# Kernel tuning notes

Measured on AMD Instinct MI355X. Metric: run time of the kernel, lower is better.

## Reference

```python
import jax, jax.numpy as jnp
import numpy as np

D_MODEL = 1024
NHEAD = 16
D_K = D_MODEL // NHEAD


def setup_inputs() -> dict:
    key = jax.random.key(0)
    ks = jax.random.split(key, 11)
    B, S = 2, 2048
    scale = 1.0 / np.sqrt(D_MODEL)
    inp = {
        "q": jax.random.normal(ks[0], (B, S, D_MODEL), jnp.float32),
        "k": jax.random.normal(ks[1], (B, S, D_MODEL), jnp.float32),
        "v": jax.random.normal(ks[2], (B, S, D_MODEL), jnp.float32),
        "Wq": jax.random.normal(ks[3], (D_MODEL, D_MODEL), jnp.float32) * scale,
        "bq": jnp.zeros((D_MODEL,), jnp.float32),
        "Wk": jax.random.normal(ks[4], (D_MODEL, D_MODEL), jnp.float32) * scale,
        "bk": jnp.zeros((D_MODEL,), jnp.float32),
        "Wv": jax.random.normal(ks[5], (D_MODEL, D_MODEL), jnp.float32) * scale,
        "bv": jnp.zeros((D_MODEL,), jnp.float32),
        "Wo": jax.random.normal(ks[6], (D_MODEL, D_MODEL), jnp.float32) * scale,
        "bo": jnp.zeros((D_MODEL,), jnp.float32),
    }
    return inp


def reference(q, k, v, Wq, bq, Wk, bk, Wv, bv, Wo, bo):
    B, S, _ = q.shape
    # Linear projections (torch Linear: x @ W.T + b), split into heads
    def proj(x, W, b):
        y = jnp.einsum('bsd,ed->bse', x, W) + b
        return y.reshape(B, -1, NHEAD, D_K).transpose(0, 2, 1, 3)  # [B,H,S,Dk]

    qh = proj(q, Wq, bq)
    kh = proj(k, Wk, bk)
    vh = proj(v, Wv, bv)

    scores = jnp.einsum('bhqd,bhkd->bhqk', qh, kh) / jnp.sqrt(
        jnp.asarray(D_K, qh.dtype))
    attn = jax.nn.softmax(scores, axis=-1)  # dropout is identity in eval
    out = jnp.einsum('bhqk,bhkd->bhqd', attn, vh)
    out = out.transpose(0, 2, 1, 3).reshape(B, S, D_MODEL)
    return jnp.einsum('bsd,ed->bse', out, Wo) + bo
```

## Files before the change

kernel.cpp:

```cpp
#include <hip/hip_runtime.h>
#include <stdint.h>
#include <stddef.h>

#define D_MODEL 1024
#define NHEAD   16
#define DK      64
#define BB      2
#define SS      2048
#define NTOK    (BB*SS)

#define SCALE_Q 0.18033688011f

typedef short  short8 __attribute__((ext_vector_type(8)));
typedef __bf16 bf16x8 __attribute__((ext_vector_type(8)));
typedef float  f32x4  __attribute__((ext_vector_type(4)));

__device__ __forceinline__ unsigned short f2bf(float x){
  unsigned int u = __builtin_bit_cast(unsigned int, x);
  u += 0x7fffu + ((u >> 16) & 1u);
  return (unsigned short)(u >> 16);
}

__device__ __forceinline__ unsigned int pack_bf2(float x, float y){
  unsigned int a = __builtin_bit_cast(unsigned int, x) + 0x8000u;
  unsigned int b = __builtin_bit_cast(unsigned int, y) + 0x8000u;
  return __builtin_amdgcn_perm(b, a, 0x07060302u);
}

__device__ __forceinline__ unsigned int cvt_pk_bf16(float lo, float hi){
  unsigned int r;
  asm("v_cvt_pk_bf16_f32 %0, %1, %2" : "=v"(r) : "v"(lo), "v"(hi));
  return r;
}

__device__ __forceinline__ float fast_exp2(float x){
#if __has_builtin(__builtin_amdgcn_exp2f)
  return __builtin_amdgcn_exp2f(x);
#else
  return exp2f(x);
#endif
}

__device__ __forceinline__ f32x4 mfma16(bf16x8 a, bf16x8 b, f32x4 c){
  return __builtin_amdgcn_mfma_f32_16x16x32_bf16(a, b, c, 0, 0, 0);
}

__device__ __forceinline__ void async16(const void* g, void* lds){
  __builtin_amdgcn_global_load_lds(
      (const __attribute__((address_space(1))) unsigned int*)g,
      (__attribute__((address_space(3))) unsigned int*)lds,
      16, 0, 0);
}

__global__ __launch_bounds__(256) void cast_bf16_all(
    const float* __restrict__ q,  const float* __restrict__ k,  const float* __restrict__ v,
    const float* __restrict__ wq, const float* __restrict__ wk, const float* __restrict__ wv,
    const float* __restrict__ wo,
    unsigned short* __restrict__ qb,  unsigned short* __restrict__ kb,  unsigned short* __restrict__ vb,
    unsigned short* __restrict__ wqb, unsigned short* __restrict__ wkb, unsigned short* __restrict__ wvb,
    unsigned short* __restrict__ wob)
{
  const float* src; unsigned short* dst; int n;
  switch (blockIdx.y){
    case 0: src = q;  dst = qb;  n = NTOK*D_MODEL;    break;
    case 1: src = k;  dst = kb;  n = NTOK*D_MODEL;    break;
    case 2: src = v;  dst = vb;  n = NTOK*D_MODEL;    break;
    case 3: src = wq; dst = wqb; n = D_MODEL*D_MODEL; break;
    case 4: src = wk; dst = wkb; n = D_MODEL*D_MODEL; break;
    case 5: src = wv; dst = wvb; n = D_MODEL*D_MODEL; break;
    default: src = wo; dst = wob; n = D_MODEL*D_MODEL; break;
  }
  int i = (blockIdx.x * 256 + threadIdx.x) * 8;
  if (i >= n) return;
  float4 a = *(const float4*)(src + i);
  float4 b = *(const float4*)(src + i + 4);
  short8 o;
  o[0] = (short)f2bf(a.x); o[1] = (short)f2bf(a.y);
  o[2] = (short)f2bf(a.z); o[3] = (short)f2bf(a.w);
  o[4] = (short)f2bf(b.x); o[5] = (short)f2bf(b.y);
  o[6] = (short)f2bf(b.z); o[7] = (short)f2bf(b.w);
  *(short8*)(dst + i) = o;
}

__global__ __launch_bounds__(256) void qkv_gemm(
    const unsigned short* __restrict__ qb, const unsigned short* __restrict__ kb,
    const unsigned short* __restrict__ vb,
    const unsigned short* __restrict__ wqb, const unsigned short* __restrict__ wkb,
    const unsigned short* __restrict__ wvb,
    const float* __restrict__ bq, const float* __restrict__ bk, const float* __restrict__ bv,
    unsigned short* __restrict__ Qh, unsigned short* __restrict__ Kh, unsigned short* __restrict__ Vt)
{
  __shared__ __align__(16) unsigned short As[128*64];
  __shared__ __align__(16) unsigned short Bs[128*64];
  const int id = blockIdx.x, z = id >> 8, r = id & 255;
  const unsigned short *A, *Bt; const float* bias; unsigned short* C;
  int bm, bn, N, brow; float scale;
  if (z == 0){ A = qb;  Bt = wqb; bias = bq; C = Qh; bm = (r>>3)*128; bn = (r&7)*128; N = 1024; brow = 0; scale = SCALE_Q; }
  else if (z == 1){ A = kb;  Bt = wkb; bias = bk; C = Kh; bm = (r>>3)*128; bn = (r&7)*128; N = 1024; brow = 0; scale = 1.0f; }
  else            { A = wvb; Bt = vb;  bias = bv; C = Vt; bm = (r&7)*128; bn = (r>>3)*128; N = 4096; brow = 1; scale = 1.0f; }
  const int K = 1024;
  const int tid  = threadIdx.x, lane = tid & 63, w = tid >> 6;
  const int quad = lane >> 4,   l16  = lane & 15;
  const int wm = w >> 1, wn = w & 1;
  const int sw = l16 & 7;
  f32x4 acc[4][4] = {};
  for (int kb_ = 0; kb_ < 16; ++kb_){
    const int k0 = kb_ << 6;
    __syncthreads();
    #pragma unroll
    for (int c = 0; c < 4; ++c){
      int chunk = (w*4 + c)*64 + lane;
      int row = chunk >> 3, c8 = chunk & 7;
      int cs = (c8 ^ (row & 7)) << 3;
      async16(A  + (size_t)(bm + row)*K + k0 + cs, (char*)As + (w*4 + c)*1024);
      async16(Bt + (size_t)(bn + row)*K + k0 + cs, (char*)Bs + (w*4 + c)*1024);
    }
    __syncthreads();
    bf16x8 af[4][2], bf[4][2];
    #pragma unroll
    for (int mt = 0; mt < 4; ++mt)
      #pragma unroll
      for (int ks = 0; ks < 2; ++ks){
        int off = (((ks*4 + quad) ^ sw) << 3);
        af[mt][ks] = *(const bf16x8*)&As[(wm*64 + mt*16 + l16)*64 + off];
        bf[mt][ks] = *(const bf16x8*)&Bs[(wn*64 + mt*16 + l16)*64 + off];
      }
    #pragma unroll
    for (int ks = 0; ks < 2; ++ks)
      #pragma unroll
      for (int mt = 0; mt < 4; ++mt)
        #pragma unroll
        for (int nt = 0; nt < 4; ++nt)
          acc[mt][nt] = mfma16(af[mt][ks], bf[nt][ks], acc[mt][nt]);
  }
  const int m0 = bm + wm*64, n0 = bn + wn*64;
  #pragma unroll
  for (int mt = 0; mt < 4; ++mt){
    #pragma unroll
    for (int nt = 0; nt < 4; ++nt){
      int col = n0 + nt*16 + l16;
      float bc = brow ? 0.0f : bias[col];
      #pragma unroll
      for (int rr = 0; rr < 4; ++rr){
        int row = m0 + mt*16 + quad*4 + rr;
        float val = (acc[mt][nt][rr] + (brow ? bias[row] : bc)) * scale;
        C[(size_t)row*N + col] = f2bf(val);
      }
    }
  }
}

__global__ __launch_bounds__(256) void gemm_out(
    const unsigned short* __restrict__ A, const unsigned short* __restrict__ Bt,
    const float* __restrict__ bias, float* __restrict__ C)
{
  __shared__ __align__(16) unsigned short As[64*64];
  __shared__ __align__(16) unsigned short Bs[128*64];
  const int K = 1024, N = 1024;
  const int tid  = threadIdx.x, lane = tid & 63, w = tid >> 6;
  const int quad = lane >> 4,   l16  = lane & 15;
  const int bm = blockIdx.y * 64, bn = blockIdx.x * 128;
  const int sw = l16 & 7;
  f32x4 acc[4][2] = {};
  for (int kb_ = 0; kb_ < 16; ++kb_){
    const int k0 = kb_ << 6;
    __syncthreads();
    #pragma unroll
    for (int c = 0; c < 2; ++c){
      int chunk = (w*2 + c)*64 + lane;
      int row = chunk >> 3, c8 = chunk & 7;
      async16(A + (size_t)(bm + row)*K + k0 + ((c8 ^ (row & 7)) << 3),
              (char*)As + (w*2 + c)*1024);
    }
    #pragma unroll
    for (int c = 0; c < 4; ++c){
      int chunk = (w*4 + c)*64 + lane;
      int row = chunk >> 3, c8 = chunk & 7;
      async16(Bt + (size_t)(bn + row)*K + k0 + ((c8 ^ (row & 7)) << 3),
              (char*)Bs + (w*4 + c)*1024);
    }
    __syncthreads();
    bf16x8 af[4][2], bf[2][2];
    #pragma unroll
    for (int mt = 0; mt < 4; ++mt)
      #pragma unroll
      for (int ks = 0; ks < 2; ++ks)
        af[mt][ks] = *(const bf16x8*)&As[(mt*16 + l16)*64 + (((ks*4 + quad) ^ sw) << 3)];
    #pragma unroll
    for (int nt = 0; nt < 2; ++nt)
      #pragma unroll
      for (int ks = 0; ks < 2; ++ks)
        bf[nt][ks] = *(const bf16x8*)&Bs[(w*32 + nt*16 + l16)*64 + (((ks*4 + quad) ^ sw) << 3)];
    #pragma unroll
    for (int ks = 0; ks < 2; ++ks)
      #pragma unroll
      for (int mt = 0; mt < 4; ++mt)
        #pragma unroll
        for (int nt = 0; nt < 2; ++nt)
          acc[mt][nt] = mfma16(af[mt][ks], bf[nt][ks], acc[mt][nt]);
  }
  #pragma unroll
  for (int mt = 0; mt < 4; ++mt){
    #pragma unroll
    for (int nt = 0; nt < 2; ++nt){
      int col = bn + w*32 + nt*16 + l16;
      float bc = bias[col];
      #pragma unroll
      for (int rr = 0; rr < 4; ++rr){
        int row = bm + mt*16 + quad*4 + rr;
        C[(size_t)row*N + col] = acc[mt][nt][rr] + bc;
      }
    }
  }
}

__global__ __launch_bounds__(256) void attn(
    const unsigned short* __restrict__ Qh, const unsigned short* __restrict__ Kh,
    const unsigned short* __restrict__ Vt, unsigned short* __restrict__ ctx)
{
  __shared__ __align__(16) unsigned short Kbuf[2][64*64];
  __shared__ __align__(16) unsigned short Vbuf[2][64*64];
  __shared__ __align__(16) unsigned short QP[128*64];

  const int tid  = threadIdx.x, lane = tid & 63, w = tid >> 6;
  const int quad = lane >> 4,   l16  = lane & 15;
  const int b = blockIdx.y >> 4, h = blockIdx.y & 15;
  const int q0 = blockIdx.x * 128;
  const int sw = l16 & 7;
  const int qh = quad >> 1, ql = (quad & 1) * 4;

  #pragma unroll
  for (int c = 0; c < 4; ++c){
    int s = (w*4 + c)*64 + lane;
    int row = s >> 3, c8 = s & 7;
    async16(Qh + (size_t)(b*SS + q0 + row)*D_MODEL + h*DK + ((c8 ^ (row & 7)) << 3),
            (char*)QP + (w*4 + c)*1024);
  }

  const unsigned short* Kp = Kh + (size_t)(b*SS)*D_MODEL + h*DK;
  const unsigned short* Vp = Vt + (size_t)(h*DK)*NTOK + b*SS;
  const unsigned short* ksrc[2];
  const unsigned short* vsrc[2];
  #pragma unroll
  for (int c = 0; c < 2; ++c){
    int s = (w*2 + c)*64 + lane;
    int row = s >> 3, c8 = s & 7;
    int cs = (c8 ^ (row & 7)) << 3;
    ksrc[c] = Kp + (size_t)row*D_MODEL + cs;
    vsrc[c] = Vp + (size_t)row*NTOK  + cs;
  }

  #pragma unroll
  for (int c = 0; c < 2; ++c){
    async16(ksrc[c], (char*)Kbuf[0] + (w*2 + c)*1024);
    async16(vsrc[c], (char*)Vbuf[0] + (w*2 + c)*1024);
    ksrc[c] += 64*D_MODEL;
    vsrc[c] += 64;
  }
  __syncthreads();

  bf16x8 bq0[2], bq1[2];
  #pragma unroll
  for (int ks = 0; ks < 2; ++ks){
    bq0[ks] = *(const bf16x8*)&QP[(w*32 +      l16)*64 + (((ks*4 + quad) ^ sw) << 3)];
    bq1[ks] = *(const bf16x8*)&QP[(w*32 + 16 + l16)*64 + (((ks*4 + quad) ^ sw) << 3)];
  }

  f32x4 acc[2][4] = {};
  float l_i[2] = {0.0f, 0.0f};

  for (int it = 0; it < 32; ++it){
    const int cur = it & 1;
    #pragma unroll
    for (int c = 0; c < 2; ++c){
      async16(ksrc[c], (char*)Kbuf[1 - cur] + (w*2 + c)*1024);
      async16(vsrc[c], (char*)Vbuf[1 - cur] + (w*2 + c)*1024);
      ksrc[c] += 64*D_MODEL;
      vsrc[c] += 64;
    }
    asm volatile("s_waitcnt vmcnt(4)\n\ts_barrier" ::: "memory");

    const unsigned short* Kc = Kbuf[cur];
    const unsigned short* Vc = Vbuf[cur];

    bf16x8 kf[4][2];
    #pragma unroll
    for (int mt = 0; mt < 4; ++mt)
      #pragma unroll
      for (int ks = 0; ks < 2; ++ks)
        kf[mt][ks] = *(const bf16x8*)&Kc[(mt*16 + l16)*64 + (((ks*4 + quad) ^ sw) << 3)];

    uint2 vfr[4][2][2];
    #pragma unroll
    for (int nt = 0; nt < 4; ++nt)
      #pragma unroll
      for (int ks = 0; ks < 2; ++ks){
        int rb = (nt*16 + l16)*64 + ql;
        vfr[nt][ks][0] = *(const uint2*)&Vc[rb + (((ks*4     + qh) ^ sw) << 3)];
        vfr[nt][ks][1] = *(const uint2*)&Vc[rb + (((ks*4 + 2 + qh) ^ sw) << 3)];
      }

    f32x4 s0[4] = {}, s1[4] = {};
    #pragma unroll
    for (int mt = 0; mt < 4; ++mt)
      #pragma unroll
      for (int ks = 0; ks < 2; ++ks){
        s0[mt] = mfma16(kf[mt][ks], bq0[ks], s0[mt]);
        s1[mt] = mfma16(kf[mt][ks], bq1[ks], s1[mt]);
      }

    float ls0 = 0.0f, ls1 = 0.0f;
    #pragma unroll
    for (int mt = 0; mt < 4; ++mt)
      #pragma unroll
      for (int rr = 0; rr < 4; ++rr){
        float p0 = fast_exp2(s0[mt][rr]); s0[mt][rr] = p0; ls0 += p0;
        float p1 = fast_exp2(s1[mt][rr]); s1[mt][rr] = p1; ls1 += p1;
      }
    l_i[0] += ls0; l_i[1] += ls1;

    bf16x8 bp0[2], bp1[2];
    #pragma unroll
    for (int ks = 0; ks < 2; ++ks){
      uint4 t;
      t.x = cvt_pk_bf16(s0[2*ks  ][0], s0[2*ks  ][1]);
      t.y = cvt_pk_bf16(s0[2*ks  ][2], s0[2*ks  ][3]);
      t.z = cvt_pk_bf16(s0[2*ks+1][0], s0[2*ks+1][1]);
      t.w = cvt_pk_bf16(s0[2*ks+1][2], s0[2*ks+1][3]);
      bp0[ks] = __builtin_bit_cast(bf16x8, t);
      t.x = cvt_pk_bf16(s1[2*ks  ][0], s1[2*ks  ][1]);
      t.y = cvt_pk_bf16(s1[2*ks  ][2], s1[2*ks  ][3]);
      t.z = cvt_pk_bf16(s1[2*ks+1][0], s1[2*ks+1][1]);
      t.w = cvt_pk_bf16(s1[2*ks+1][2], s1[2*ks+1][3]);
      bp1[ks] = __builtin_bit_cast(bf16x8, t);
    }

    #pragma unroll
    for (int nt = 0; nt < 4; ++nt)
      #pragma unroll
      for (int ks = 0; ks < 2; ++ks){
        uint4 vv;
        vv.x = vfr[nt][ks][0].x; vv.y = vfr[nt][ks][0].y;
        vv.z = vfr[nt][ks][1].x; vv.w = vfr[nt][ks][1].y;
        bf16x8 vf = __builtin_bit_cast(bf16x8, vv);
        acc[0][nt] = mfma16(vf, bp0[ks], acc[0][nt]);
        acc[1][nt] = mfma16(vf, bp1[ks], acc[1][nt]);
      }

    asm volatile("s_waitcnt lgkmcnt(0)\n\ts_barrier" ::: "memory");
  }

  float inv[2];
  #pragma unroll
  for (int qg = 0; qg < 2; ++qg){
    float t = l_i[qg];
    t += __shfl_xor(t, 16);
    t += __shfl_xor(t, 32);
    inv[qg] = 1.0f / t;
  }
  #pragma unroll
  for (int qg = 0; qg < 2; ++qg){
    int pr = (w*32 + qg*16 + l16)*64;
    #pragma unroll
    for (int nt = 0; nt < 4; ++nt){
      int c8  = nt*2 + (quad >> 1);
      int off = ((c8 ^ sw) << 3) + (quad & 1)*4;
      uint2 p;
      p.x = pack_bf2(acc[qg][nt][0]*inv[qg], acc[qg][nt][1]*inv[qg]);
      p.y = pack_bf2(acc[qg][nt][2]*inv[qg], acc[qg][nt][3]*inv[qg]);
      *(uint2*)&QP[pr + off] = p;
    }
  }
  asm volatile("s_waitcnt lgkmcnt(0)" ::: "memory");
  {
    int r  = w*32 + (lane >> 1);
    int j0 = (lane & 1)*4;
    unsigned short* dst = ctx + (size_t)(b*SS + q0 + r)*D_MODEL + h*DK;
    #pragma unroll
    for (int i = 0; i < 4; ++i){
      int j = j0 + i;
      uint4 d = *(const uint4*)&QP[r*64 + ((j ^ (r & 7)) << 3)];
      *(uint4*)(dst + j*8) = d;
    }
  }
}

extern "C" void kernel_launch(void* const* d_in, const int* in_sizes, int n_in,
                              void* d_out, int out_size, void* d_ws, size_t ws_size,
                              hipStream_t stream) {
  const float* q  = (const float*)d_in[0];
  const float* k  = (const float*)d_in[1];
  const float* v  = (const float*)d_in[2];
  const float* Wq = (const float*)d_in[3];
  const float* bq = (const float*)d_in[4];
  const float* Wk = (const float*)d_in[5];
  const float* bk = (const float*)d_in[6];
  const float* Wv = (const float*)d_in[7];
  const float* bv = (const float*)d_in[8];
  const float* Wo = (const float*)d_in[9];
  const float* bo = (const float*)d_in[10];

  char* ws = (char*)d_ws;
  const size_t TOKB = (size_t)NTOK * D_MODEL * 2;
  const size_t WB   = (size_t)D_MODEL * D_MODEL * 2;
  unsigned short* qb  = (unsigned short*)ws;             ws += TOKB;
  unsigned short* kb  = (unsigned short*)ws;             ws += TOKB;
  unsigned short* vb  = (unsigned short*)ws;             ws += TOKB;
  unsigned short* wqb = (unsigned short*)ws;             ws += WB;
  unsigned short* wkb = (unsigned short*)ws;             ws += WB;
  unsigned short* wvb = (unsigned short*)ws;             ws += WB;
  unsigned short* wob = (unsigned short*)ws;             ws += WB;
  unsigned short* Qh  = (unsigned short*)ws;             ws += TOKB;
  unsigned short* Kh  = (unsigned short*)ws;             ws += TOKB;
  unsigned short* Vt  = (unsigned short*)ws;             ws += TOKB;
  unsigned short* ctx = (unsigned short*)ws;             ws += TOKB;

  cast_bf16_all<<<dim3(2048, 7), 256, 0, stream>>>(q, k, v, Wq, Wk, Wv, Wo,
                                                   qb, kb, vb, wqb, wkb, wvb, wob);
  qkv_gemm<<<dim3(768), 256, 0, stream>>>(qb, kb, vb, wqb, wkb, wvb,
                                          bq, bk, bv, Qh, Kh, Vt);
  attn<<<dim3(SS/128, BB*NHEAD), 256, 0, stream>>>(Qh, Kh, Vt, ctx);
  gemm_out<<<dim3(8, 64), 256, 0, stream>>>(ctx, wob, bo, (float*)d_out);
}
```

Baseline: 239.6 us.

## Double KV tile to 128 keys per stage with new V swizzle and MFMA priority

Each pipeline stage of the attention kernel now loads 128 keys instead of 64 and processes them as two halves, cutting the main loop to 16 iterations. This halves the barriers and waitcnt stalls per key. The V buffer layout and its XOR swizzle are reworked for 128-wide rows. The MFMA sections are wrapped in s_setprio, and the row-sum accumulators are split to shorten dependency chains. The cost is double the LDS use for K/V buffers, which may reduce occupancy.

```diff
diff --git a/kernel.cpp b/kernel.cpp
--- a/kernel.cpp
+++ b/kernel.cpp
@@ -218,16 +218,16 @@
     const unsigned short* __restrict__ Qh, const unsigned short* __restrict__ Kh,
     const unsigned short* __restrict__ Vt, unsigned short* __restrict__ ctx)
 {
-  __shared__ __align__(16) unsigned short Kbuf[2][64*64];
-  __shared__ __align__(16) unsigned short Vbuf[2][64*64];
+  __shared__ __align__(16) unsigned short Kbuf[2][128*64];
+  __shared__ __align__(16) unsigned short Vbuf[2][64*128];
   __shared__ __align__(16) unsigned short QP[128*64];
 
   const int tid  = threadIdx.x, lane = tid & 63, w = tid >> 6;
   const int quad = lane >> 4,   l16  = lane & 15;
   const int b = blockIdx.y >> 4, h = blockIdx.y & 15;
   const int q0 = blockIdx.x * 128;
-  const int sw = l16 & 7;
-  const int qh = quad >> 1, ql = (quad & 1) * 4;
+  const int sw   = l16 & 7;
+  const int vkey = l16 & 14;
 
   #pragma unroll
   for (int c = 0; c < 4; ++c){
@@ -239,23 +239,23 @@
 
   const unsigned short* Kp = Kh + (size_t)(b*SS)*D_MODEL + h*DK;
   const unsigned short* Vp = Vt + (size_t)(h*DK)*NTOK + b*SS;
-  const unsigned short* ksrc[2];
-  const unsigned short* vsrc[2];
-  #pragma unroll
-  for (int c = 0; c < 2; ++c){
-    int s = (w*2 + c)*64 + lane;
-    int row = s >> 3, c8 = s & 7;
-    int cs = (c8 ^ (row & 7)) << 3;
-    ksrc[c] = Kp + (size_t)row*D_MODEL + cs;
-    vsrc[c] = Vp + (size_t)row*NTOK  + cs;
-  }
-
-  #pragma unroll
-  for (int c = 0; c < 2; ++c){
-    async16(ksrc[c], (char*)Kbuf[0] + (w*2 + c)*1024);
-    async16(vsrc[c], (char*)Vbuf[0] + (w*2 + c)*1024);
-    ksrc[c] += 64*D_MODEL;
-    vsrc[c] += 64;
+  const unsigned short* ksrc[4];
+  const unsigned short* vsrc[4];
+  #pragma unroll
+  for (int c = 0; c < 4; ++c){
+    int s = (w*4 + c)*64 + lane;
+    int kr = s >> 3, kc8 = s & 7;
+    ksrc[c] = Kp + (size_t)kr*D_MODEL + ((kc8 ^ (kr & 7)) << 3);
+    int vr = s >> 4, vc16 = s & 15;
+    vsrc[c] = Vp + (size_t)vr*NTOK + ((vc16 ^ ((vr >> 1) & 7)) << 3);
+  }
+
+  #pragma unroll
+  for (int c = 0; c < 4; ++c){
+    async16(ksrc[c], (char*)Kbuf[0] + (w*4 + c)*1024);
+    async16(vsrc[c], (char*)Vbuf[0] + (w*4 + c)*1024);
+    ksrc[c] += 128*D_MODEL;
+    vsrc[c] += 128;
   }
   __syncthreads();
 
@@ -267,89 +267,99 @@
   }
 
   f32x4 acc[2][4] = {};
-  float l_i[2] = {0.0f, 0.0f};
-
-  for (int it = 0; it < 32; ++it){
+  float l0a = 0.0f, l0b = 0.0f, l1a = 0.0f, l1b = 0.0f;
+
+  for (int it = 0; it < 16; ++it){
     const int cur = it & 1;
     #pragma unroll
-    for (int c = 0; c < 2; ++c){
-      async16(ksrc[c], (char*)Kbuf[1 - cur] + (w*2 + c)*1024);
-      async16(vsrc[c], (char*)Vbuf[1 - cur] + (w*2 + c)*1024);
-      ksrc[c] += 64*D_MODEL;
-      vsrc[c] += 64;
-    }
-    asm volatile("s_waitcnt vmcnt(4)\n\ts_barrier" ::: "memory");
+    for (int c = 0; c < 4; ++c){
+      async16(ksrc[c], (char*)Kbuf[1 - cur] + (w*4 + c)*1024);
+      async16(vsrc[c], (char*)Vbuf[1 - cur] + (w*4 + c)*1024);
+      ksrc[c] += 128*D_MODEL;
+      vsrc[c] += 128;
+    }
+    asm volatile("s_waitcnt vmcnt(8)\n\ts_barrier" ::: "memory");
 
     const unsigned short* Kc = Kbuf[cur];
     const unsigned short* Vc = Vbuf[cur];
 
-    bf16x8 kf[4][2];
-    #pragma unroll
-    for (int mt = 0; mt < 4; ++mt)
-      #pragma unroll
-      for (int ks = 0; ks < 2; ++ks)
-        kf[mt][ks] = *(const bf16x8*)&Kc[(mt*16 + l16)*64 + (((ks*4 + quad) ^ sw) << 3)];
-
-    uint2 vfr[4][2][2];
-    #pragma unroll
-    for (int nt = 0; nt < 4; ++nt)
-      #pragma unroll
-      for (int ks = 0; ks < 2; ++ks){
-        int rb = (nt*16 + l16)*64 + ql;
-        vfr[nt][ks][0] = *(const uint2*)&Vc[rb + (((ks*4     + qh) ^ sw) << 3)];
-        vfr[nt][ks][1] = *(const uint2*)&Vc[rb + (((ks*4 + 2 + qh) ^ sw) << 3)];
+    #pragma unroll
+    for (int half = 0; half < 2; ++half){
+      bf16x8 kf[4][2];
+      #pragma unroll
+      for (int mt = 0; mt < 4; ++mt)
+        #pragma unroll
+        for (int ks = 0; ks < 2; ++ks)
+          kf[mt][ks] = *(const bf16x8*)&Kc[(half*64 + mt*16 + l16)*64 + (((ks*4 + quad) ^ sw) << 3)];
+
+      uint2 vfr[4][2][2];
+      #pragma unroll
+      for (int nt = 0; nt < 4; ++nt)
+        #pragma unroll
+        for (int kss = 0; kss < 2; ++kss){
+          int rb = (nt*16 + l16)*128;
+          int hd = 8*(2*half + kss) + quad;
+          vfr[nt][kss][0] = *(const uint2*)&Vc[rb + (((hd    ) ^ vkey) << 2)];
+          vfr[nt][kss][1] = *(const uint2*)&Vc[rb + (((hd + 4) ^ vkey) << 2)];
+        }
+
+      f32x4 s0[4] = {}, s1[4] = {};
+      __builtin_amdgcn_s_setprio(1);
+      #pragma unroll
+      for (int mt = 0; mt < 4; ++mt)
+        #pragma unroll
+        for (int ks = 0; ks < 2; ++ks){
+          s0[mt] = mfma16(kf[mt][ks], bq0[ks], s0[mt]);
+          s1[mt] = mfma16(kf[mt][ks], bq1[ks], s1[mt]);
+        }
+      __builtin_amdgcn_s_setprio(0);
+
+      float s0a = 0.0f, s0b = 0.0f, s1a = 0.0f, s1b = 0.0f;
+      #pragma unroll
+      for (int mt = 0; mt < 4; ++mt)
+        #pragma unroll
+        for (int rr = 0; rr < 4; ++rr){
+          float p0 = fast_exp2(s0[mt][rr]); s0[mt][rr] = p0;
+          float p1 = fast_exp2(s1[mt][rr]); s1[mt][rr] = p1;
+          if (mt & 1){ s0b += p0; s1b += p1; } else { s0a += p0; s1a += p1; }
+        }
+      l0a += s0a; l0b += s0b; l1a += s1a; l1b += s1b;
+
+      bf16x8 bp0[2], bp1[2];
+      #pragma unroll
+      for (int kss = 0; kss < 2; ++kss){
+        uint4 t;
+        t.x = cvt_pk_bf16(s0[2*kss  ][0], s0[2*kss  ][1]);
+        t.y = cvt_pk_bf16(s0[2*kss  ][2], s0[2*kss  ][3]);
+        t.z = cvt_pk_bf16(s0[2*kss+1][0], s0[2*kss+1][1]);
+        t.w = cvt_pk_bf16(s0[2*kss+1][2], s0[2*kss+1][3]);
+        bp0[kss] = __builtin_bit_cast(bf16x8, t);
+        t.x = cvt_pk_bf16(s1[2*kss  ][0], s1[2*kss  ][1]);
+        t.y = cvt_pk_bf16(s1[2*kss  ][2], s1[2*kss  ][3]);
+        t.z = cvt_pk_bf16(s1[2*kss+1][0], s1[2*kss+1][1]);
+        t.w = cvt_pk_bf16(s1[2*kss+1][2], s1[2*kss+1][3]);
+        bp1[kss] = __builtin_bit_cast(bf16x8, t);
       }
 
-    f32x4 s0[4] = {}, s1[4] = {};
-    #pragma unroll
-    for (int mt = 0; mt < 4; ++mt)
-      #pragma unroll
-      for (int ks = 0; ks < 2; ++ks){
-        s0[mt] = mfma16(kf[mt][ks], bq0[ks], s0[mt]);
-        s1[mt] = mfma16(kf[mt][ks], bq1[ks], s1[mt]);
-      }
-
-    float ls0 = 0.0f, ls1 = 0.0f;
-    #pragma unroll
-    for (int mt = 0; mt < 4; ++mt)
-      #pragma unroll
-      for (int rr = 0; rr < 4; ++rr){
-        float p0 = fast_exp2(s0[mt][rr]); s0[mt][rr] = p0; ls0 += p0;
-        float p1 = fast_exp2(s1[mt][rr]); s1[mt][rr] = p1; ls1 += p1;
-      }
-    l_i[0] += ls0; l_i[1] += ls1;
-
-    bf16x8 bp0[2], bp1[2];
-    #pragma unroll
-    for (int ks = 0; ks < 2; ++ks){
-      uint4 t;
-      t.x = cvt_pk_bf16(s0[2*ks  ][0], s0[2*ks  ][1]);
-      t.y = cvt_pk_bf16(s0[2*ks  ][2], s0[2*ks  ][3]);
-      t.z = cvt_pk_bf16(s0[2*ks+1][0], s0[2*ks+1][1]);
-      t.w = cvt_pk_bf16(s0[2*ks+1][2], s0[2*ks+1][3]);
-      bp0[ks] = __builtin_bit_cast(bf16x8, t);
-      t.x = cvt_pk_bf16(s1[2*ks  ][0], s1[2*ks  ][1]);
-      t.y = cvt_pk_bf16(s1[2*ks  ][2], s1[2*ks  ][3]);
-      t.z = cvt_pk_bf16(s1[2*ks+1][0], s1[2*ks+1][1]);
-      t.w = cvt_pk_bf16(s1[2*ks+1][2], s1[2*ks+1][3]);
-      bp1[ks] = __builtin_bit_cast(bf16x8, t);
-    }
-
-    #pragma unroll
-    for (int nt = 0; nt < 4; ++nt)
-      #pragma unroll
-      for (int ks = 0; ks < 2; ++ks){
-        uint4 vv;
-        vv.x = vfr[nt][ks][0].x; vv.y = vfr[nt][ks][0].y;
-        vv.z = vfr[nt][ks][1].x; vv.w = vfr[nt][ks][1].y;
-        bf16x8 vf = __builtin_bit_cast(bf16x8, vv);
-        acc[0][nt] = mfma16(vf, bp0[ks], acc[0][nt]);
-        acc[1][nt] = mfma16(vf, bp1[ks], acc[1][nt]);
-      }
+      __builtin_amdgcn_s_setprio(1);
+      #pragma unroll
+      for (int nt = 0; nt < 4; ++nt)
+        #pragma unroll
+        for (int kss = 0; kss < 2; ++kss){
+          uint4 vv;
+          vv.x = vfr[nt][kss][0].x; vv.y = vfr[nt][kss][0].y;
+          vv.z = vfr[nt][kss][1].x; vv.w = vfr[nt][kss][1].y;
+          bf16x8 vf = __builtin_bit_cast(bf16x8, vv);
+          acc[0][nt] = mfma16(vf, bp0[kss], acc[0][nt]);
+          acc[1][nt] = mfma16(vf, bp1[kss], acc[1][nt]);
+        }
+      __builtin_amdgcn_s_setprio(0);
+    }
 
     asm volatile("s_waitcnt lgkmcnt(0)\n\ts_barrier" ::: "memory");
   }
 
+  float l_i[2] = { l0a + l0b, l1a + l1b };
   float inv[2];
   #pragma unroll
   for (int qg = 0; qg < 2; ++qg){
```

Result: faster. 232.1 us (-3.1%).

## Software-pipeline attention loop: overlap next tile's QK^T with current softmax and PV

Applied to the files above, without the earlier changes.

Restructures the attention inner loop into two stages with double-buffered register sets. Stage one does the LDS reads of K/V, issues the async prefetch and the QK^T MFMAs for tile t+1. Stage two does exp, bf16 pack and the PV MFMAs for tile t, interleaved with stage one. The aim is to hide MFMA latency and the exp/convert work behind independent matrix work, and to cut per-iteration barrier stalls. The row-sum accumulators are also split into two partial sums to shorten the dependency chain. The cost is much higher VGPR pressure from holding two score and V-fragment sets, which may reduce occupancy or cause spills. The wait before each stage is now vmcnt(0) instead of a partial count.

```diff
diff --git a/kernel.cpp b/kernel.cpp
--- a/kernel.cpp
+++ b/kernel.cpp
@@ -257,7 +257,7 @@
     ksrc[c] += 64*D_MODEL;
     vsrc[c] += 64;
   }
-  __syncthreads();
+  asm volatile("s_waitcnt vmcnt(0)\n\ts_barrier" ::: "memory");
 
   bf16x8 bq0[2], bq1[2];
   #pragma unroll
@@ -267,58 +267,57 @@
   }
 
   f32x4 acc[2][4] = {};
-  float l_i[2] = {0.0f, 0.0f};
-
-  for (int it = 0; it < 32; ++it){
-    const int cur = it & 1;
+  float l0a = 0.0f, l0b = 0.0f, l1a = 0.0f, l1b = 0.0f;
+
+  auto readstage = [&](int it, f32x4 (&so0)[4], f32x4 (&so1)[4],
+                       uint2 (&vfo)[4][2][2]){
+    asm volatile("s_waitcnt vmcnt(0)\n\ts_barrier" ::: "memory");
+    const unsigned short* Kc = Kbuf[it & 1];
+    const unsigned short* Vc = Vbuf[it & 1];
+    bf16x8 kf[4][2];
+    #pragma unroll
+    for (int mt = 0; mt < 4; ++mt)
+      #pragma unroll
+      for (int ks = 0; ks < 2; ++ks)
+        kf[mt][ks] = *(const bf16x8*)&Kc[(mt*16 + l16)*64 + (((ks*4 + quad) ^ sw) << 3)];
+    #pragma unroll
+    for (int nt = 0; nt < 4; ++nt)
+      #pragma unroll
+      for (int ks = 0; ks < 2; ++ks){
+        int rb = (nt*16 + l16)*64 + ql;
+        vfo[nt][ks][0] = *(const uint2*)&Vc[rb + (((ks*4     + qh) ^ sw) << 3)];
+        vfo[nt][ks][1] = *(const uint2*)&Vc[rb + (((ks*4 + 2 + qh) ^ sw) << 3)];
+      }
     #pragma unroll
     for (int c = 0; c < 2; ++c){
-      async16(ksrc[c], (char*)Kbuf[1 - cur] + (w*2 + c)*1024);
-      async16(vsrc[c], (char*)Vbuf[1 - cur] + (w*2 + c)*1024);
+      async16(ksrc[c], (char*)Kbuf[1 - (it & 1)] + (w*2 + c)*1024);
+      async16(vsrc[c], (char*)Vbuf[1 - (it & 1)] + (w*2 + c)*1024);
       ksrc[c] += 64*D_MODEL;
       vsrc[c] += 64;
     }
-    asm volatile("s_waitcnt vmcnt(4)\n\ts_barrier" ::: "memory");
-
-    const unsigned short* Kc = Kbuf[cur];
-    const unsigned short* Vc = Vbuf[cur];
-
-    bf16x8 kf[4][2];
+    #pragma unroll
+    for (int mt = 0; mt < 4; ++mt){
+      f32x4 a0 = {}, a1 = {};
+      #pragma unroll
+      for (int ks = 0; ks < 2; ++ks){
+        a0 = mfma16(kf[mt][ks], bq0[ks], a0);
+        a1 = mfma16(kf[mt][ks], bq1[ks], a1);
+      }
+      so0[mt] = a0; so1[mt] = a1;
+    }
+  };
+
+  auto smpv = [&](f32x4 (&s0)[4], f32x4 (&s1)[4], uint2 (&vfr)[4][2][2]){
+    float s0a = 0.0f, s0b = 0.0f, s1a = 0.0f, s1b = 0.0f;
     #pragma unroll
     for (int mt = 0; mt < 4; ++mt)
       #pragma unroll
-      for (int ks = 0; ks < 2; ++ks)
-        kf[mt][ks] = *(const bf16x8*)&Kc[(mt*16 + l16)*64 + (((ks*4 + quad) ^ sw) << 3)];
-
-    uint2 vfr[4][2][2];
-    #pragma unroll
-    for (int nt = 0; nt < 4; ++nt)
-      #pragma unroll
-      for (int ks = 0; ks < 2; ++ks){
-        int rb = (nt*16 + l16)*64 + ql;
-        vfr[nt][ks][0] = *(const uint2*)&Vc[rb + (((ks*4     + qh) ^ sw) << 3)];
-        vfr[nt][ks][1] = *(const uint2*)&Vc[rb + (((ks*4 + 2 + qh) ^ sw) << 3)];
-      }
-
-    f32x4 s0[4] = {}, s1[4] = {};
-    #pragma unroll
-    for (int mt = 0; mt < 4; ++mt)
-      #pragma unroll
-      for (int ks = 0; ks < 2; ++ks){
-        s0[mt] = mfma16(kf[mt][ks], bq0[ks], s0[mt]);
-        s1[mt] = mfma16(kf[mt][ks], bq1[ks], s1[mt]);
-      }
-
-    float ls0 = 0.0f, ls1 = 0.0f;
-    #pragma unroll
-    for (int mt = 0; mt < 4; ++mt)
-      #pragma unroll
       for (int rr = 0; rr < 4; ++rr){
-        float p0 = fast_exp2(s0[mt][rr]); s0[mt][rr] = p0; ls0 += p0;
-        float p1 = fast_exp2(s1[mt][rr]); s1[mt][rr] = p1; ls1 += p1;
-      }
-    l_i[0] += ls0; l_i[1] += ls1;
-
+        float p0 = fast_exp2(s0[mt][rr]); s0[mt][rr] = p0;
+        float p1 = fast_exp2(s1[mt][rr]); s1[mt][rr] = p1;
+        if (mt & 1){ s0b += p0; s1b += p1; } else { s0a += p0; s1a += p1; }
+      }
+    l0a += s0a; l0b += s0b; l1a += s1a; l1b += s1b;
     bf16x8 bp0[2], bp1[2];
     #pragma unroll
     for (int ks = 0; ks < 2; ++ks){
@@ -334,7 +333,6 @@
       t.w = cvt_pk_bf16(s1[2*ks+1][2], s1[2*ks+1][3]);
       bp1[ks] = __builtin_bit_cast(bf16x8, t);
     }
-
     #pragma unroll
     for (int nt = 0; nt < 4; ++nt)
       #pragma unroll
@@ -346,10 +344,20 @@
         acc[0][nt] = mfma16(vf, bp0[ks], acc[0][nt]);
         acc[1][nt] = mfma16(vf, bp1[ks], acc[1][nt]);
       }
-
-    asm volatile("s_waitcnt lgkmcnt(0)\n\ts_barrier" ::: "memory");
-  }
-
+  };
+
+  f32x4 sA0[4], sA1[4], sB0[4], sB1[4];
+  uint2 vA[4][2][2], vB[4][2][2];
+
+  readstage(0, sA0, sA1, vA);
+  for (int t = 1; t < 31; t += 2){
+    readstage(t,     sB0, sB1, vB);  smpv(sA0, sA1, vA);
+    readstage(t + 1, sA0, sA1, vA);  smpv(sB0, sB1, vB);
+  }
+  readstage(31, sB0, sB1, vB);  smpv(sA0, sA1, vA);
+  smpv(sB0, sB1, vB);
+
+  float l_i[2] = { l0a + l0b, l1a + l1b };
   float inv[2];
   #pragma unroll
   for (int qg = 0; qg < 2; ++qg){
```

Measured after the change: 243.3 us. About the same (+1.6%).

## Pre-permute V-transpose columns in projection epilogue to allow 16-byte V fragment loads

Applied to the files above, without the earlier changes.

The projection GEMM epilogue for the transposed-V output (brow path) now writes columns in a permuted order within each 32-token group. This lets the attention kernel read V fragments as single 16-byte LDS loads matching the K/Q pattern instead of two 8-byte loads that were stitched together. The row-sum accumulation is also split into two partial chains per query group to shorten the dependent add chain. The result depends on the permutation matching the P fragment's k ordering exactly; a mismatch would silently give wrong outputs.

```diff
diff --git a/kernel.cpp b/kernel.cpp
--- a/kernel.cpp
+++ b/kernel.cpp
@@ -139,12 +139,15 @@
     #pragma unroll
     for (int nt = 0; nt < 4; ++nt){
       int col = n0 + nt*16 + l16;
+      int scol = brow ? ((col & ~31) | (((col >> 2) & 3) << 3)
+                                    | (((col >> 4) & 1) << 2) | (col & 3))
+                      : col;
       float bc = brow ? 0.0f : bias[col];
       #pragma unroll
       for (int rr = 0; rr < 4; ++rr){
         int row = m0 + mt*16 + quad*4 + rr;
         float val = (acc[mt][nt][rr] + (brow ? bias[row] : bc)) * scale;
-        C[(size_t)row*N + col] = f2bf(val);
+        C[(size_t)row*N + scol] = f2bf(val);
       }
     }
   }
@@ -227,7 +230,6 @@
   const int b = blockIdx.y >> 4, h = blockIdx.y & 15;
   const int q0 = blockIdx.x * 128;
   const int sw = l16 & 7;
-  const int qh = quad >> 1, ql = (quad & 1) * 4;
 
   #pragma unroll
   for (int c = 0; c < 4; ++c){
@@ -267,7 +269,7 @@
   }
 
   f32x4 acc[2][4] = {};
-  float l_i[2] = {0.0f, 0.0f};
+  float l0a = 0.0f, l0b = 0.0f, l1a = 0.0f, l1b = 0.0f;
 
   for (int it = 0; it < 32; ++it){
     const int cur = it & 1;
@@ -290,15 +292,12 @@
       for (int ks = 0; ks < 2; ++ks)
         kf[mt][ks] = *(const bf16x8*)&Kc[(mt*16 + l16)*64 + (((ks*4 + quad) ^ sw) << 3)];
 
-    uint2 vfr[4][2][2];
+    bf16x8 vf[4][2];
     #pragma unroll
     for (int nt = 0; nt < 4; ++nt)
       #pragma unroll
-      for (int ks = 0; ks < 2; ++ks){
-        int rb = (nt*16 + l16)*64 + ql;
-        vfr[nt][ks][0] = *(const uint2*)&Vc[rb + (((ks*4     + qh) ^ sw) << 3)];
-        vfr[nt][ks][1] = *(const uint2*)&Vc[rb + (((ks*4 + 2 + qh) ^ sw) << 3)];
-      }
+      for (int ks = 0; ks < 2; ++ks)
+        vf[nt][ks] = *(const bf16x8*)&Vc[(nt*16 + l16)*64 + (((ks*4 + quad) ^ sw) << 3)];
 
     f32x4 s0[4] = {}, s1[4] = {};
     #pragma unroll
@@ -309,15 +308,16 @@
         s1[mt] = mfma16(kf[mt][ks], bq1[ks], s1[mt]);
       }
 
-    float ls0 = 0.0f, ls1 = 0.0f;
+    float s0a = 0.0f, s0b = 0.0f, s1a = 0.0f, s1b = 0.0f;
     #pragma unroll
     for (int mt = 0; mt < 4; ++mt)
       #pragma unroll
       for (int rr = 0; rr < 4; ++rr){
-        float p0 = fast_exp2(s0[mt][rr]); s0[mt][rr] = p0; ls0 += p0;
-        float p1 = fast_exp2(s1[mt][rr]); s1[mt][rr] = p1; ls1 += p1;
-      }
-    l_i[0] += ls0; l_i[1] += ls1;
+        float p0 = fast_exp2(s0[mt][rr]); s0[mt][rr] = p0;
+        float p1 = fast_exp2(s1[mt][rr]); s1[mt][rr] = p1;
+        if (mt & 1){ s0b += p0; s1b += p1; } else { s0a += p0; s1a += p1; }
+      }
+    l0a += s0a; l0b += s0b; l1a += s1a; l1b += s1b;
 
     bf16x8 bp0[2], bp1[2];
     #pragma unroll
@@ -339,17 +339,14 @@
     for (int nt = 0; nt < 4; ++nt)
       #pragma unroll
       for (int ks = 0; ks < 2; ++ks){
-        uint4 vv;
-        vv.x = vfr[nt][ks][0].x; vv.y = vfr[nt][ks][0].y;
-        vv.z = vfr[nt][ks][1].x; vv.w = vfr[nt][ks][1].y;
-        bf16x8 vf = __builtin_bit_cast(bf16x8, vv);
-        acc[0][nt] = mfma16(vf, bp0[ks], acc[0][nt]);
-        acc[1][nt] = mfma16(vf, bp1[ks], acc[1][nt]);
+        acc[0][nt] = mfma16(vf[nt][ks], bp0[ks], acc[0][nt]);
+        acc[1][nt] = mfma16(vf[nt][ks], bp1[ks], acc[1][nt]);
       }
 
     asm volatile("s_waitcnt lgkmcnt(0)\n\ts_barrier" ::: "memory");
   }
 
+  float l_i[2] = { l0a + l0b, l1a + l1b };
   float inv[2];
   #pragma unroll
   for (int qg = 0; qg < 2; ++qg){
```

Measured after the change: 238.3 us. No clear change (-0.5%).
